# Performance work log

Hardware: AMD Instinct MI355X
Metric: run time of the kernel (lower is better)

The kernel has to match this reference:

```python
import jax, jax.numpy as jnp
import numpy as np

ROLE_BITS = 20
NHEAD = 16
D_MODEL = 1024
D_KEY = D_MODEL // NHEAD  # 64
D_FIL = 512
DFF = 4096
EPS = 1e-5


def _ln(x, g, b):
    mu = jnp.mean(x, axis=-1, keepdims=True)
    var = jnp.mean(jnp.square(x - mu), axis=-1, keepdims=True)
    return (x - mu) * jax.lax.rsqrt(var + EPS) * g + b


def setup_inputs() -> dict:
    key = jax.random.key(0)
    ks = jax.random.split(key, 10)
    N, BSZ, MEM = 16384, 16, 8
    D_IN = D_FIL + ROLE_BITS  # 532
    values = jax.random.normal(ks[0], (N, D_FIL), jnp.float32)
    role_index = jax.random.randint(ks[1], (N,), 1, 2 ** ROLE_BITS)
    # every (batch, memory_slot) pair occupied -> static shapes (compression is a no-op)
    slot = jax.random.permutation(ks[2], jnp.tile(jnp.arange(BSZ * MEM), N // (BSZ * MEM)))
    batch_index = (slot // MEM).astype(jnp.int32)
    memory_index = (slot % MEM).astype(jnp.int32)
    query_vectors = jax.random.normal(ks[3], (NHEAD, D_KEY), jnp.float32) * (1.0 / np.sqrt(D_KEY))
    s = 0.02
    Wk = jax.random.normal(ks[4], (D_MODEL, D_IN), jnp.float32) * s
    Wv = jax.random.normal(ks[5], (D_MODEL, D_IN), jnp.float32) * s
    Wo = jax.random.normal(ks[6], (D_MODEL, D_MODEL), jnp.float32) * s
    W1 = jax.random.normal(ks[7], (DFF, D_MODEL), jnp.float32) * s
    W2 = jax.random.normal(ks[8], (D_MODEL, DFF), jnp.float32) * s
    return dict(
        values=values, role_index=role_index, batch_index=batch_index,
        memory_index=memory_index, query_vectors=query_vectors,
        Wk=Wk, Wv=Wv, Wo=Wo, bo=jnp.zeros((D_MODEL,), jnp.float32),
        W1=W1, b1=jnp.zeros((DFF,), jnp.float32),
        W2=W2, b2=jnp.zeros((D_MODEL,), jnp.float32),
        g_fil=jnp.ones((D_FIL,), jnp.float32), b_fil=jnp.zeros((D_FIL,), jnp.float32),
        g_mha=jnp.ones((D_IN,), jnp.float32), b_mha=jnp.zeros((D_IN,), jnp.float32),
        g_ff=jnp.ones((D_MODEL,), jnp.float32), b_ff=jnp.zeros((D_MODEL,), jnp.float32),
        g_out=jnp.ones((D_MODEL,), jnp.float32), b_out=jnp.zeros((D_MODEL,), jnp.float32),
        bsz=BSZ, memory_slots=MEM,
    )


def _tree_positional_encodings(role_index):
    # bit-expand role indices: column j is bit j of the role index
    bits = (jnp.bitwise_and(role_index[:, None], 2 ** jnp.arange(ROLE_BITS)) != 0).astype(jnp.float32)
    # locate the highest set bit (torch: flip + argmax)
    mi = jnp.argmax(bits[:, ::-1], axis=1)
    cm = ROLE_BITS - 1 - mi  # index of highest set bit
    bits = bits * (1.0 - jax.nn.one_hot(cm, ROLE_BITS, dtype=bits.dtype))  # zero it out
    branch = jnp.arange(ROLE_BITS)[None, :] < cm[:, None]
    return jnp.where(branch, (bits - 0.5) * 2.0, bits)  # {0,1} -> {-1,1} below MSB


def reference(values, role_index, batch_index, memory_index, query_vectors,
              Wk, Wv, Wo, bo, W1, b1, W2, b2,
              g_fil, b_fil, g_mha, b_mha, g_ff, b_ff, g_out, b_out,
              bsz, memory_slots):
    N = values.shape[0]
    T = bsz * memory_slots  # num_trees (all (batch, slot) pairs occupied)

    tpd = _tree_positional_encodings(role_index)
    x = jnp.concatenate([_ln(values, g_fil, b_fil), tpd], axis=1)  # [N, d_input]
    x = _ln(x, g_mha, b_mha)
    k = (x @ Wk.T).reshape(N, NHEAD, D_KEY)
    v = (x @ Wv.T).reshape(N, NHEAD, D_KEY)
    qkm = jnp.einsum('nhd,hd->nh', k, query_vectors)  # [N, H]

    # combined batch+memory mask: node n attends to flat tree t = b*mem + m
    node_slot = batch_index * memory_slots + memory_index  # [N]
    mask = node_slot[:, None] == jnp.arange(T)[None, :]  # [N, T]
    scores = jnp.where(mask[:, :, None], qkm[:, None, :], -1e9) / np.sqrt(D_KEY)
    attn = jax.nn.softmax(scores, axis=0)  # softmax over nodes, [N, T, H]
    out = jnp.einsum('nhv,nth->thv', v, attn).reshape(T, D_MODEL)

    # post-attention: proj_o + residual with flattened queries, LN, FF, LN
    r1 = (out @ Wo.T + bo) + query_vectors.reshape(-1)
    l1 = _ln(r1, g_ff, b_ff)
    ff = jax.nn.gelu(l1 @ W1.T + b1, approximate=False) @ W2.T + b2
    l2 = _ln(ff + r1, g_out, b_out)

    rectangle_out = l2.reshape(bsz, memory_slots, D_MODEL)
    agent_pad_mask = jnp.zeros((bsz, memory_slots), dtype=bool)
    return rectangle_out, agent_pad_mask
```

## Files before the change

kernel.cpp:

```cpp
#include <hip/hip_runtime.h>
#include <hip/hip_bf16.h>

typedef __hip_bfloat16 bf16;

#define N_NODES 16384
#define D_FIL 512
#define D_IN 532
#define D_MODEL 1024
#define NHEAD 16
#define D_KEY 64
#define DFF 4096
#define NTREE 128
#define MEM_SLOTS 8
#define NODES_PER_TREE 128
#define EPS 1e-5f
#define XSE 544
#define XSU 272
#define CSTR 32
#define BSTR 40

typedef float f32x4 __attribute__((ext_vector_type(4)));
typedef short s16x8 __attribute__((ext_vector_type(8)));

union PackU { uint4 u; s16x8 s; };

__device__ inline float gelu_exact(float x) {
    return 0.5f * x * (1.0f + erff(x * 0.7071067811865476f));
}

__device__ inline void blockReduceSum2(float& a, float& b, float* sm) {
    int tid = threadIdx.x;
    int lane = tid & 63, wid = tid >> 6;
#pragma unroll
    for (int off = 32; off > 0; off >>= 1) {
        a += __shfl_down(a, off, 64);
        b += __shfl_down(b, off, 64);
    }
    if (lane == 0) { sm[wid] = a; sm[4 + wid] = b; }
    __syncthreads();
    if (tid == 0) {
        sm[8] = sm[0] + sm[1] + sm[2] + sm[3];
        sm[9] = sm[4] + sm[5] + sm[6] + sm[7];
    }
    __syncthreads();
    a = sm[8]; b = sm[9];
}

__global__ __launch_bounds__(256) void prep_kernel(
        const float* __restrict__ values, const int* __restrict__ role,
        const int* __restrict__ bidx, const int* __restrict__ midx,
        const float* __restrict__ g_fil, const float* __restrict__ b_fil,
        const float* __restrict__ g_mha, const float* __restrict__ b_mha,
        bf16* __restrict__ xs, int* __restrict__ counts,
        const float* __restrict__ q, const float* __restrict__ Wk,
        unsigned* __restrict__ wqb,
        const float* __restrict__ Wv, float* __restrict__ wvt) {
    int b = blockIdx.x;
    int tid = threadIdx.x;

    if (b < 16) {
        int h = b;
        __shared__ float qs[64];
        if (tid < 64) qs[tid] = q[h * 64 + tid];
        __syncthreads();
        for (int p = tid; p < XSU; p += 256) {
            unsigned out = 0u;
            if (p < 266) {
                float a0 = 0.f, a1 = 0.f;
                int j0 = 2 * p;
#pragma unroll 8
                for (int d = 0; d < 64; ++d) {
                    const float* wr = Wk + (size_t)(h * 64 + d) * D_IN;
                    a0 += qs[d] * wr[j0];
                    a1 += qs[d] * wr[j0 + 1];
                }
                unsigned u0 = (unsigned)__bfloat16_as_ushort(__float2bfloat16(a0));
                unsigned u1 = (unsigned)__bfloat16_as_ushort(__float2bfloat16(a1));
                out = (u1 << 16) | u0;
            }
            wqb[h * XSU + p] = out;
        }
        return;
    }

    if (b < 560) {
        __shared__ float tile[32][33];
        int vb = b - 16;
        int c0 = (vb & 31) * 32, j0 = (vb >> 5) * 32;
        int tx = tid & 31, ty = tid >> 5;
#pragma unroll
        for (int r = 0; r < 4; ++r) {
            int cc = ty + r * 8;
            int j = j0 + tx;
            tile[cc][tx] = (j < D_IN) ? Wv[(size_t)(c0 + cc) * D_IN + j] : 0.f;
        }
        __syncthreads();
#pragma unroll
        for (int r = 0; r < 4; ++r) {
            int j = j0 + ty + r * 8;
            if (j < D_IN) wvt[(size_t)j * D_MODEL + c0 + tx] = tile[tx][ty + r * 8];
        }
        return;
    }

    int wave = tid >> 6;
    int l = tid & 63;
    int n = (b - 560) * 4 + wave;

    const float4* vp = (const float4*)(values + (size_t)n * D_FIL + l * 8);
    float4 v0 = vp[0], v1 = vp[1];

    int row = 0;
    if (l == 0) {
        int slot = bidx[n] * MEM_SLOTS + midx[n];
        int pos = atomicAdd(&counts[slot * CSTR], 1);
        row = slot * NODES_PER_TREE + pos;
    }

    float s = v0.x + v0.y + v0.z + v0.w + v1.x + v1.y + v1.z + v1.w;
    float ss = v0.x * v0.x + v0.y * v0.y + v0.z * v0.z + v0.w * v0.w
             + v1.x * v1.x + v1.y * v1.y + v1.z * v1.z + v1.w * v1.w;
#pragma unroll
    for (int m = 1; m < 64; m <<= 1) {
        s += __shfl_xor(s, m, 64);
        ss += __shfl_xor(ss, m, 64);
    }
    float mu = s * (1.f / D_FIL);
    float var = ss * (1.f / D_FIL) - mu * mu;
    float rs = rsqrtf(var + EPS);

    const float4* gf = (const float4*)(g_fil + l * 8);
    const float4* bf = (const float4*)(b_fil + l * 8);
    float4 gf0 = gf[0], gf1 = gf[1], bf0 = bf[0], bf1 = bf[1];
    float y[8];
    y[0] = (v0.x - mu) * rs * gf0.x + bf0.x;
    y[1] = (v0.y - mu) * rs * gf0.y + bf0.y;
    y[2] = (v0.z - mu) * rs * gf0.z + bf0.z;
    y[3] = (v0.w - mu) * rs * gf0.w + bf0.w;
    y[4] = (v1.x - mu) * rs * gf1.x + bf1.x;
    y[5] = (v1.y - mu) * rs * gf1.y + bf1.y;
    y[6] = (v1.z - mu) * rs * gf1.z + bf1.z;
    y[7] = (v1.w - mu) * rs * gf1.w + bf1.w;

    int r = role[n];
    int cm = 31 - __clz(r);
    float s_t = 2.f * (float)(__popc(r) - 1) - (float)cm;
    float ss_t = (float)cm;

    float s2 = y[0] + y[1] + y[2] + y[3] + y[4] + y[5] + y[6] + y[7];
    float ss2 = y[0] * y[0] + y[1] * y[1] + y[2] * y[2] + y[3] * y[3]
              + y[4] * y[4] + y[5] * y[5] + y[6] * y[6] + y[7] * y[7];
#pragma unroll
    for (int m = 1; m < 64; m <<= 1) {
        s2 += __shfl_xor(s2, m, 64);
        ss2 += __shfl_xor(ss2, m, 64);
    }
    s2 += s_t; ss2 += ss_t;
    float mu2 = s2 * (1.f / D_IN);
    float var2 = ss2 * (1.f / D_IN) - mu2 * mu2;
    float rs2 = rsqrtf(var2 + EPS);

    const float4* gm = (const float4*)(g_mha + l * 8);
    const float4* bm = (const float4*)(b_mha + l * 8);
    float4 gm0 = gm[0], gm1 = gm[1], bm0 = bm[0], bm1 = bm[1];
    float x[8];
    x[0] = (y[0] - mu2) * rs2 * gm0.x + bm0.x;
    x[1] = (y[1] - mu2) * rs2 * gm0.y + bm0.y;
    x[2] = (y[2] - mu2) * rs2 * gm0.z + bm0.z;
    x[3] = (y[3] - mu2) * rs2 * gm0.w + bm0.w;
    x[4] = (y[4] - mu2) * rs2 * gm1.x + bm1.x;
    x[5] = (y[5] - mu2) * rs2 * gm1.y + bm1.y;
    x[6] = (y[6] - mu2) * rs2 * gm1.z + bm1.z;
    x[7] = (y[7] - mu2) * rs2 * gm1.w + bm1.w;

    row = __shfl(row, 0, 64);

    {
        unsigned us[8];
#pragma unroll
        for (int k = 0; k < 8; ++k)
            us[k] = (unsigned)__bfloat16_as_ushort(__float2bfloat16(x[k]));
        uint4 pk = make_uint4((us[1] << 16) | us[0], (us[3] << 16) | us[2],
                              (us[5] << 16) | us[4], (us[7] << 16) | us[6]);
        *(uint4*)((char*)xs + (size_t)row * (XSE * 2) + 16 * l) = pk;
    }

    if (l < 20) {
        int bit = (r >> l) & 1;
        float tpd = (l < cm) ? (bit ? 1.f : -1.f) : 0.f;
        float x2 = (tpd - mu2) * rs2 * g_mha[512 + l] + b_mha[512 + l];
        xs[(size_t)row * XSE + 512 + l] = __float2bfloat16(x2);
    } else if (l < 26) {
        ((unsigned*)xs)[(size_t)row * XSU + 266 + (l - 20)] = 0u;
    }
}

__global__ __launch_bounds__(256) void qkm_kernel(const unsigned* __restrict__ xsu,
                                                  const unsigned* __restrict__ wqb,
                                                  float* __restrict__ qkmp) {
    __shared__ unsigned wshw[16 * 274];
    int tid = threadIdx.x;
#pragma unroll
    for (int hh = 0; hh < 16; ++hh) {
        wshw[hh * 274 + tid] = wqb[hh * XSU + tid];
        if (tid < 16) wshw[hh * 274 + 256 + tid] = wqb[hh * XSU + 256 + tid];
    }
    __syncthreads();

    int h = tid & 15, rp = tid >> 4;
    int r0 = blockIdx.x * 32;
    const uint2* xr0 = (const uint2*)(xsu + (size_t)(r0 + 2 * rp) * XSU);
    const uint2* xr1 = (const uint2*)(xsu + (size_t)(r0 + 2 * rp + 1) * XSU);
    const uint2* wr  = (const uint2*)(wshw + h * 274);
    float a0 = 0.f, a1 = 0.f;
#pragma unroll 8
    for (int j = 0; j < 136; ++j) {
        uint2 wu = wr[j];
        uint2 xa = xr0[j];
        uint2 xb = xr1[j];
        float w0 = __uint_as_float(wu.x << 16), w1 = __uint_as_float(wu.x & 0xffff0000u);
        float w2 = __uint_as_float(wu.y << 16), w3 = __uint_as_float(wu.y & 0xffff0000u);
        a0 += __uint_as_float(xa.x << 16) * w0 + __uint_as_float(xa.x & 0xffff0000u) * w1
            + __uint_as_float(xa.y << 16) * w2 + __uint_as_float(xa.y & 0xffff0000u) * w3;
        a1 += __uint_as_float(xb.x << 16) * w0 + __uint_as_float(xb.x & 0xffff0000u) * w1
            + __uint_as_float(xb.y << 16) * w2 + __uint_as_float(xb.y & 0xffff0000u) * w3;
    }
    qkmp[(size_t)(r0 + 2 * rp) * NHEAD + h] = a0;
    qkmp[(size_t)(r0 + 2 * rp + 1) * NHEAD + h] = a1;
}

__global__ void attn_fused_kernel(const float* __restrict__ qkmp, const unsigned* __restrict__ xsu,
                                  const float* __restrict__ wvt, float* __restrict__ attn_out) {
    int hg = blockIdx.x, t = blockIdx.y, tid = threadIdx.x;
    __shared__ __align__(16) float a4[NODES_PER_TREE * 4];
    __shared__ float zs[4][536];

    for (int l = tid; l < NODES_PER_TREE * 4; l += 256) {
        int i = l >> 2, hh = l & 3;
        a4[l] = qkmp[(size_t)t * NODES_PER_TREE * NHEAD + i * 16 + hg * 4 + hh] * 0.125f;
    }
    __syncthreads();

    int hh = tid >> 6, lane = tid & 63;
    {
        float s0 = a4[lane * 4 + hh], s1 = a4[(lane + 64) * 4 + hh];
        float m = fmaxf(s0, s1);
#pragma unroll
        for (int off = 32; off > 0; off >>= 1) m = fmaxf(m, __shfl_xor(m, off, 64));
        float e0 = expf(s0 - m), e1 = expf(s1 - m);
        float sum = e0 + e1;
#pragma unroll
        for (int off = 32; off > 0; off >>= 1) sum += __shfl_xor(sum, off, 64);
        float inv = 1.0f / sum;
        a4[lane * 4 + hh] = e0 * inv;
        a4[(lane + 64) * 4 + hh] = e1 * inv;
    }
    __syncthreads();

    {
        bool hasT = tid < 10;
        float az[4][2] = {};
        float at[4][2] = {};
        const unsigned* xt = xsu + (size_t)t * NODES_PER_TREE * XSU;
        for (int i0 = 0; i0 < NODES_PER_TREE; i0 += 8) {
            unsigned u[8], u2[8];
            float4 av[8];
#pragma unroll
            for (int k = 0; k < 8; ++k) u[k] = xt[(size_t)(i0 + k) * XSU + tid];
#pragma unroll
            for (int k = 0; k < 8; ++k) u2[k] = hasT ? xt[(size_t)(i0 + k) * XSU + 256 + tid] : 0u;
#pragma unroll
            for (int k = 0; k < 8; ++k) av[k] = *(const float4*)(a4 + (i0 + k) * 4);
#pragma unroll
            for (int k = 0; k < 8; ++k) {
                float x0 = __uint_as_float(u[k] << 16);
                float x1 = __uint_as_float(u[k] & 0xffff0000u);
                float x2 = __uint_as_float(u2[k] << 16);
                float x3 = __uint_as_float(u2[k] & 0xffff0000u);
                float4 a = av[k];
                az[0][0] += a.x * x0; az[0][1] += a.x * x1;
                az[1][0] += a.y * x0; az[1][1] += a.y * x1;
                az[2][0] += a.z * x0; az[2][1] += a.z * x1;
                az[3][0] += a.w * x0; az[3][1] += a.w * x1;
                at[0][0] += a.x * x2; at[0][1] += a.x * x3;
                at[1][0] += a.y * x2; at[1][1] += a.y * x3;
                at[2][0] += a.z * x2; at[2][1] += a.z * x3;
                at[3][0] += a.w * x2; at[3][1] += a.w * x3;
            }
        }
#pragma unroll
        for (int k = 0; k < 4; ++k) {
            *(float2*)(&zs[k][2 * tid]) = make_float2(az[k][0], az[k][1]);
            if (hasT) *(float2*)(&zs[k][512 + 2 * tid]) = make_float2(at[k][0], at[k][1]);
        }
    }
    __syncthreads();

    int c = hg * 256 + tid;
    const float* wp = wvt + c;
    float acc0 = 0.f, acc1 = 0.f;
    for (int j0 = 0; j0 < 528; j0 += 8) {
        float wv[8];
#pragma unroll
        for (int k = 0; k < 8; ++k) wv[k] = wp[(size_t)(j0 + k) * D_MODEL];
#pragma unroll
        for (int k = 0; k < 8; k += 2) {
            acc0 += zs[hh][j0 + k] * wv[k];
            acc1 += zs[hh][j0 + k + 1] * wv[k + 1];
        }
    }
    {
        float wv[4];
#pragma unroll
        for (int k = 0; k < 4; ++k) wv[k] = wp[(size_t)(528 + k) * D_MODEL];
#pragma unroll
        for (int k = 0; k < 4; k += 2) {
            acc0 += zs[hh][528 + k] * wv[k];
            acc1 += zs[hh][528 + k + 1] * wv[k + 1];
        }
    }
    attn_out[(size_t)t * D_MODEL + c] = acc0 + acc1;
}

__global__ __launch_bounds__(256) void gemm_mfma_sk(const float* __restrict__ A,
                                                    const float* __restrict__ B,
                                                    float* __restrict__ Cpart,
                                                    int N, int K, int nsb) {
    __shared__ __align__(16) unsigned short bhi[64 * BSTR];
    __shared__ __align__(16) unsigned short blo[64 * BSTR];
    int tid = threadIdx.x;
    int col0 = blockIdx.x * 64;
    int k0 = blockIdx.y * nsb * 32;
    float* C = Cpart + (size_t)blockIdx.y * 128 * N;

    int w = tid >> 6, l = tid & 63;
    int l15 = l & 15, l4 = l >> 4;
    int scol = tid >> 2, sk8 = (tid & 3) * 8;

    f32x4 acc[2][4];
#pragma unroll
    for (int rt = 0; rt < 2; ++rt)
#pragma unroll
        for (int ct = 0; ct < 4; ++ct) acc[rt][ct] = (f32x4){0.f, 0.f, 0.f, 0.f};

    for (int s = 0; s < nsb; ++s) {
        int kb = k0 + s * 32;

        {
            const float* bp = B + (size_t)(col0 + scol) * K + kb + sk8;
            float4 f0 = *(const float4*)bp;
            float4 f1 = *(const float4*)(bp + 4);
            float fe[8] = {f0.x, f0.y, f0.z, f0.w, f1.x, f1.y, f1.z, f1.w};
            unsigned hu[4], lu[4];
#pragma unroll
            for (int p = 0; p < 4; ++p) {
                unsigned u0 = __float_as_uint(fe[2 * p]);
                unsigned u1 = __float_as_uint(fe[2 * p + 1]);
                unsigned h0 = u0 & 0xffff0000u, h1 = u1 & 0xffff0000u;
                float d0 = fe[2 * p] - __uint_as_float(h0);
                float d1 = fe[2 * p + 1] - __uint_as_float(h1);
                hu[p] = h1 | (u0 >> 16);
                lu[p] = (__float_as_uint(d1) & 0xffff0000u) | (__float_as_uint(d0) >> 16);
            }
            *(uint4*)(&bhi[scol * BSTR + sk8]) = make_uint4(hu[0], hu[1], hu[2], hu[3]);
            *(uint4*)(&blo[scol * BSTR + sk8]) = make_uint4(lu[0], lu[1], lu[2], lu[3]);
        }
        __syncthreads();

        s16x8 ah[2], al[2];
#pragma unroll
        for (int rt = 0; rt < 2; ++rt) {
            const float* ap = A + (size_t)(32 * w + 16 * rt + l15) * K + kb + l4 * 8;
            float4 f0 = *(const float4*)ap;
            float4 f1 = *(const float4*)(ap + 4);
            float fe[8] = {f0.x, f0.y, f0.z, f0.w, f1.x, f1.y, f1.z, f1.w};
            unsigned hu[4], lu[4];
#pragma unroll
            for (int p = 0; p < 4; ++p) {
                unsigned u0 = __float_as_uint(fe[2 * p]);
                unsigned u1 = __float_as_uint(fe[2 * p + 1]);
                unsigned h0 = u0 & 0xffff0000u, h1 = u1 & 0xffff0000u;
                float d0 = fe[2 * p] - __uint_as_float(h0);
                float d1 = fe[2 * p + 1] - __uint_as_float(h1);
                hu[p] = h1 | (u0 >> 16);
                lu[p] = (__float_as_uint(d1) & 0xffff0000u) | (__float_as_uint(d0) >> 16);
            }
            PackU uh, ul;
            uh.u = make_uint4(hu[0], hu[1], hu[2], hu[3]);
            ul.u = make_uint4(lu[0], lu[1], lu[2], lu[3]);
            ah[rt] = uh.s;
            al[rt] = ul.s;
        }

#pragma unroll
        for (int ct = 0; ct < 4; ++ct) {
            PackU rbh, rbl;
            rbh.u = *(const uint4*)(&bhi[(16 * ct + l15) * BSTR + l4 * 8]);
            rbl.u = *(const uint4*)(&blo[(16 * ct + l15) * BSTR + l4 * 8]);
#pragma unroll
            for (int rt = 0; rt < 2; ++rt) {
                acc[rt][ct] = __builtin_amdgcn_mfma_f32_16x16x32_bf16(ah[rt], rbh.s, acc[rt][ct], 0, 0, 0);
                acc[rt][ct] = __builtin_amdgcn_mfma_f32_16x16x32_bf16(al[rt], rbh.s, acc[rt][ct], 0, 0, 0);
                acc[rt][ct] = __builtin_amdgcn_mfma_f32_16x16x32_bf16(ah[rt], rbl.s, acc[rt][ct], 0, 0, 0);
            }
        }
        __syncthreads();
    }

#pragma unroll
    for (int rt = 0; rt < 2; ++rt) {
        int row = 32 * w + 16 * rt + l4 * 4;
#pragma unroll
        for (int ct = 0; ct < 4; ++ct) {
            int col = col0 + 16 * ct + l15;
#pragma unroll
            for (int r = 0; r < 4; ++r)
                C[(size_t)(row + r) * N + col] = acc[rt][ct][r];
        }
    }
}

__global__ void ln_r1_kernel(const float* __restrict__ po, const float* __restrict__ bo,
                             const float* __restrict__ qvec, const float* __restrict__ g,
                             const float* __restrict__ b, float* __restrict__ r1,
                             float* __restrict__ l1) {
    int t = blockIdx.x, tid = threadIdx.x;
    __shared__ float sm[16];
    float e[4];
#pragma unroll
    for (int c = 0; c < 4; ++c) {
        int j = c * 256 + tid;
        float v = bo[j] + qvec[j];
#pragma unroll
        for (int s = 0; s < 8; ++s)
            v += po[(size_t)s * NTREE * D_MODEL + (size_t)t * D_MODEL + j];
        e[c] = v;
        r1[(size_t)t * D_MODEL + j] = v;
    }
    float s = e[0] + e[1] + e[2] + e[3];
    float ss = e[0] * e[0] + e[1] * e[1] + e[2] * e[2] + e[3] * e[3];
    blockReduceSum2(s, ss, sm);
    float mu = s * (1.f / D_MODEL);
    float var = ss * (1.f / D_MODEL) - mu * mu;
    float rs = rsqrtf(var + EPS);
#pragma unroll
    for (int c = 0; c < 4; ++c) {
        int j = c * 256 + tid;
        l1[(size_t)t * D_MODEL + j] = (e[c] - mu) * rs * g[j] + b[j];
    }
}

__global__ void gelu_reduce_kernel(const float* __restrict__ p1, const float* __restrict__ b1,
                                   float* __restrict__ h1) {
    int idx4 = (blockIdx.x * 256 + threadIdx.x) * 4;
    int col = idx4 & (DFF - 1);
    float4 v = *(const float4*)(b1 + col);
#pragma unroll
    for (int s = 0; s < 4; ++s) {
        float4 p = *(const float4*)(p1 + (size_t)s * NTREE * DFF + idx4);
        v.x += p.x; v.y += p.y; v.z += p.z; v.w += p.w;
    }
    v.x = gelu_exact(v.x); v.y = gelu_exact(v.y);
    v.z = gelu_exact(v.z); v.w = gelu_exact(v.w);
    *(float4*)(h1 + idx4) = v;
}

__global__ void ln_out_kernel(const float* __restrict__ p2, const float* __restrict__ b2,
                              const float* __restrict__ r1, const float* __restrict__ g,
                              const float* __restrict__ b, float* __restrict__ out) {
    int t = blockIdx.x, tid = threadIdx.x;
    __shared__ float sm[16];
    float e[4];
#pragma unroll
    for (int c = 0; c < 4; ++c) {
        int j = c * 256 + tid;
        float v = b2[j] + r1[(size_t)t * D_MODEL + j];
#pragma unroll
        for (int s = 0; s < 16; ++s)
            v += p2[(size_t)s * NTREE * D_MODEL + (size_t)t * D_MODEL + j];
        e[c] = v;
    }
    float s = e[0] + e[1] + e[2] + e[3];
    float ss = e[0] * e[0] + e[1] * e[1] + e[2] * e[2] + e[3] * e[3];
    blockReduceSum2(s, ss, sm);
    float mu = s * (1.f / D_MODEL);
    float var = ss * (1.f / D_MODEL) - mu * mu;
    float rs = rsqrtf(var + EPS);
#pragma unroll
    for (int c = 0; c < 4; ++c) {
        int j = c * 256 + tid;
        out[(size_t)t * D_MODEL + j] = (e[c] - mu) * rs * g[j] + b[j];
    }
    if (t == 0 && tid < 128) out[(size_t)NTREE * D_MODEL + tid] = 0.f;
}

extern "C" void kernel_launch(void* const* d_in, const int* in_sizes, int n_in,
                              void* d_out, int out_size, void* d_ws, size_t ws_size,
                              hipStream_t stream) {
    const float* values = (const float*)d_in[0];
    const int* role     = (const int*)d_in[1];
    const int* bidx     = (const int*)d_in[2];
    const int* midx     = (const int*)d_in[3];
    const float* qvec   = (const float*)d_in[4];
    const float* Wk     = (const float*)d_in[5];
    const float* Wv     = (const float*)d_in[6];
    const float* Wo     = (const float*)d_in[7];
    const float* bo     = (const float*)d_in[8];
    const float* W1     = (const float*)d_in[9];
    const float* b1     = (const float*)d_in[10];
    const float* W2     = (const float*)d_in[11];
    const float* b2     = (const float*)d_in[12];
    const float* g_fil  = (const float*)d_in[13];
    const float* b_fil  = (const float*)d_in[14];
    const float* g_mha  = (const float*)d_in[15];
    const float* b_mha  = (const float*)d_in[16];
    const float* g_ff   = (const float*)d_in[17];
    const float* b_ff   = (const float*)d_in[18];
    const float* g_out  = (const float*)d_in[19];
    const float* b_out  = (const float*)d_in[20];

    char* w = (char*)d_ws;
    unsigned* wqb   = (unsigned*)(w + 0);
    float* qkmp     = (float*)(w + 18432);
    float* attn_out = (float*)(w + 1068032);
    float* r1       = (float*)(w + 1592320);
    float* l1       = (float*)(w + 2116608);
    float* h1       = (float*)(w + 2640896);
    int*   counts   = (int*)  (w + 2640896);
    float* wvt      = (float*)(w + 4738048);
    char*  big      = w + 6917120;
    bf16*  xs = (bf16*)big;
    float* po = (float*)big;
    float* p1 = (float*)(big + 4194304);
    float* p2 = (float*)big;

    float* out = (float*)d_out;

    hipMemsetAsync(counts, 0, 128 * CSTR * sizeof(int), stream);

    prep_kernel<<<4656, 256, 0, stream>>>(values, role, bidx, midx,
                                          g_fil, b_fil, g_mha, b_mha,
                                          xs, counts,
                                          qvec, Wk, wqb, Wv, wvt);

    qkm_kernel<<<N_NODES / 32, 256, 0, stream>>>((const unsigned*)xs, wqb, qkmp);

    attn_fused_kernel<<<dim3(4, NTREE), 256, 0, stream>>>(qkmp, (const unsigned*)xs, wvt, attn_out);

    gemm_mfma_sk<<<dim3(16, 8), 256, 0, stream>>>(attn_out, Wo, po, D_MODEL, D_MODEL, 4);

    ln_r1_kernel<<<NTREE, 256, 0, stream>>>(po, bo, qvec, g_ff, b_ff, r1, l1);

    gemm_mfma_sk<<<dim3(64, 4), 256, 0, stream>>>(l1, W1, p1, DFF, D_MODEL, 8);

    gelu_reduce_kernel<<<512, 256, 0, stream>>>(p1, b1, h1);

    gemm_mfma_sk<<<dim3(16, 16), 256, 0, stream>>>(h1, W2, p2, D_MODEL, DFF, 8);

    ln_out_kernel<<<NTREE, 256, 0, stream>>>(p2, b2, r1, g_out, b_out, out);
}
```

Baseline: 243.4 us.

## Halve GEMM column tile, double grid, hoist loads, widen LayerNorm blocks

The split-K MFMA GEMM now computes 32-column tiles instead of 64, so each of the three post-attention GEMMs launches twice as many blocks. This spreads the small M=128 GEMMs across more compute units, at the cost of reloading and re-splitting the A tile once per extra block. The A and B global loads are also issued before the bf16 hi/lo split and the LDS store, so their latency can overlap. The two LayerNorm kernels move to 512 threads per row with a matching 8-wave reduction.

```diff
diff --git a/kernel.cpp b/kernel.cpp
--- a/kernel.cpp
+++ b/kernel.cpp
@@ -28,7 +28,7 @@
     return 0.5f * x * (1.0f + erff(x * 0.7071067811865476f));
 }
 
-__device__ inline void blockReduceSum2(float& a, float& b, float* sm) {
+__device__ inline void blockReduceSum2_512(float& a, float& b, float* sm) {
     int tid = threadIdx.x;
     int lane = tid & 63, wid = tid >> 6;
 #pragma unroll
@@ -36,14 +36,16 @@
         a += __shfl_down(a, off, 64);
         b += __shfl_down(b, off, 64);
     }
-    if (lane == 0) { sm[wid] = a; sm[4 + wid] = b; }
+    if (lane == 0) { sm[wid] = a; sm[8 + wid] = b; }
     __syncthreads();
     if (tid == 0) {
-        sm[8] = sm[0] + sm[1] + sm[2] + sm[3];
-        sm[9] = sm[4] + sm[5] + sm[6] + sm[7];
+        float s0 = 0.f, s1 = 0.f;
+#pragma unroll
+        for (int i = 0; i < 8; ++i) { s0 += sm[i]; s1 += sm[8 + i]; }
+        sm[16] = s0; sm[17] = s1;
     }
     __syncthreads();
-    a = sm[8]; b = sm[9];
+    a = sm[16]; b = sm[17];
 }
 
 __global__ __launch_bounds__(256) void prep_kernel(
@@ -326,34 +328,42 @@
                                                     const float* __restrict__ B,
                                                     float* __restrict__ Cpart,
                                                     int N, int K, int nsb) {
-    __shared__ __align__(16) unsigned short bhi[64 * BSTR];
-    __shared__ __align__(16) unsigned short blo[64 * BSTR];
+    __shared__ __align__(16) unsigned short bhi[32 * BSTR];
+    __shared__ __align__(16) unsigned short blo[32 * BSTR];
     int tid = threadIdx.x;
-    int col0 = blockIdx.x * 64;
+    int col0 = blockIdx.x * 32;
     int k0 = blockIdx.y * nsb * 32;
     float* C = Cpart + (size_t)blockIdx.y * 128 * N;
 
     int w = tid >> 6, l = tid & 63;
     int l15 = l & 15, l4 = l >> 4;
-    int scol = tid >> 2, sk8 = (tid & 3) * 8;
-
-    f32x4 acc[2][4];
+    int scol = tid >> 3, sk4 = (tid & 7) * 4;
+
+    f32x4 acc[2][2];
 #pragma unroll
     for (int rt = 0; rt < 2; ++rt)
 #pragma unroll
-        for (int ct = 0; ct < 4; ++ct) acc[rt][ct] = (f32x4){0.f, 0.f, 0.f, 0.f};
+        for (int ct = 0; ct < 2; ++ct) acc[rt][ct] = (f32x4){0.f, 0.f, 0.f, 0.f};
 
     for (int s = 0; s < nsb; ++s) {
         int kb = k0 + s * 32;
 
+        const float* bp = B + (size_t)(col0 + scol) * K + kb + sk4;
+        float4 fb = *(const float4*)bp;
+
+        float4 fa[2][2];
+#pragma unroll
+        for (int rt = 0; rt < 2; ++rt) {
+            const float* ap = A + (size_t)(32 * w + 16 * rt + l15) * K + kb + l4 * 8;
+            fa[rt][0] = *(const float4*)ap;
+            fa[rt][1] = *(const float4*)(ap + 4);
+        }
+
         {
-            const float* bp = B + (size_t)(col0 + scol) * K + kb + sk8;
-            float4 f0 = *(const float4*)bp;
-            float4 f1 = *(const float4*)(bp + 4);
-            float fe[8] = {f0.x, f0.y, f0.z, f0.w, f1.x, f1.y, f1.z, f1.w};
-            unsigned hu[4], lu[4];
-#pragma unroll
-            for (int p = 0; p < 4; ++p) {
+            float fe[4] = {fb.x, fb.y, fb.z, fb.w};
+            unsigned hu[2], lu[2];
+#pragma unroll
+            for (int p = 0; p < 2; ++p) {
                 unsigned u0 = __float_as_uint(fe[2 * p]);
                 unsigned u1 = __float_as_uint(fe[2 * p + 1]);
                 unsigned h0 = u0 & 0xffff0000u, h1 = u1 & 0xffff0000u;
@@ -362,18 +372,16 @@
                 hu[p] = h1 | (u0 >> 16);
                 lu[p] = (__float_as_uint(d1) & 0xffff0000u) | (__float_as_uint(d0) >> 16);
             }
-            *(uint4*)(&bhi[scol * BSTR + sk8]) = make_uint4(hu[0], hu[1], hu[2], hu[3]);
-            *(uint4*)(&blo[scol * BSTR + sk8]) = make_uint4(lu[0], lu[1], lu[2], lu[3]);
+            *(uint2*)(&bhi[scol * BSTR + sk4]) = make_uint2(hu[0], hu[1]);
+            *(uint2*)(&blo[scol * BSTR + sk4]) = make_uint2(lu[0], lu[1]);
         }
         __syncthreads();
 
         s16x8 ah[2], al[2];
 #pragma unroll
         for (int rt = 0; rt < 2; ++rt) {
-            const float* ap = A + (size_t)(32 * w + 16 * rt + l15) * K + kb + l4 * 8;
-            float4 f0 = *(const float4*)ap;
-            float4 f1 = *(const float4*)(ap + 4);
-            float fe[8] = {f0.x, f0.y, f0.z, f0.w, f1.x, f1.y, f1.z, f1.w};
+            float fe[8] = {fa[rt][0].x, fa[rt][0].y, fa[rt][0].z, fa[rt][0].w,
+                           fa[rt][1].x, fa[rt][1].y, fa[rt][1].z, fa[rt][1].w};
             unsigned hu[4], lu[4];
 #pragma unroll
             for (int p = 0; p < 4; ++p) {
@@ -393,7 +401,7 @@
         }
 
 #pragma unroll
-        for (int ct = 0; ct < 4; ++ct) {
+        for (int ct = 0; ct < 2; ++ct) {
             PackU rbh, rbl;
             rbh.u = *(const uint4*)(&bhi[(16 * ct + l15) * BSTR + l4 * 8]);
             rbl.u = *(const uint4*)(&blo[(16 * ct + l15) * BSTR + l4 * 8]);
@@ -411,7 +419,7 @@
     for (int rt = 0; rt < 2; ++rt) {
         int row = 32 * w + 16 * rt + l4 * 4;
 #pragma unroll
-        for (int ct = 0; ct < 4; ++ct) {
+        for (int ct = 0; ct < 2; ++ct) {
             int col = col0 + 16 * ct + l15;
 #pragma unroll
             for (int r = 0; r < 4; ++r)
@@ -420,16 +428,16 @@
     }
 }
 
-__global__ void ln_r1_kernel(const float* __restrict__ po, const float* __restrict__ bo,
+__global__ __launch_bounds__(512) void ln_r1_kernel(const float* __restrict__ po, const float* __restrict__ bo,
                              const float* __restrict__ qvec, const float* __restrict__ g,
                              const float* __restrict__ b, float* __restrict__ r1,
                              float* __restrict__ l1) {
     int t = blockIdx.x, tid = threadIdx.x;
-    __shared__ float sm[16];
-    float e[4];
-#pragma unroll
-    for (int c = 0; c < 4; ++c) {
-        int j = c * 256 + tid;
+    __shared__ float sm[18];
+    float e[2];
+#pragma unroll
+    for (int c = 0; c < 2; ++c) {
+        int j = c * 512 + tid;
         float v = bo[j] + qvec[j];
 #pragma unroll
         for (int s = 0; s < 8; ++s)
@@ -437,15 +445,15 @@
         e[c] = v;
         r1[(size_t)t * D_MODEL + j] = v;
     }
-    float s = e[0] + e[1] + e[2] + e[3];
-    float ss = e[0] * e[0] + e[1] * e[1] + e[2] * e[2] + e[3] * e[3];
-    blockReduceSum2(s, ss, sm);
+    float s = e[0] + e[1];
+    float ss = e[0] * e[0] + e[1] * e[1];
+    blockReduceSum2_512(s, ss, sm);
     float mu = s * (1.f / D_MODEL);
     float var = ss * (1.f / D_MODEL) - mu * mu;
     float rs = rsqrtf(var + EPS);
 #pragma unroll
-    for (int c = 0; c < 4; ++c) {
-        int j = c * 256 + tid;
+    for (int c = 0; c < 2; ++c) {
+        int j = c * 512 + tid;
         l1[(size_t)t * D_MODEL + j] = (e[c] - mu) * rs * g[j] + b[j];
     }
 }
@@ -465,30 +473,30 @@
     *(float4*)(h1 + idx4) = v;
 }
 
-__global__ void ln_out_kernel(const float* __restrict__ p2, const float* __restrict__ b2,
+__global__ __launch_bounds__(512) void ln_out_kernel(const float* __restrict__ p2, const float* __restrict__ b2,
                               const float* __restrict__ r1, const float* __restrict__ g,
                               const float* __restrict__ b, float* __restrict__ out) {
     int t = blockIdx.x, tid = threadIdx.x;
-    __shared__ float sm[16];
-    float e[4];
-#pragma unroll
-    for (int c = 0; c < 4; ++c) {
-        int j = c * 256 + tid;
+    __shared__ float sm[18];
+    float e[2];
+#pragma unroll
+    for (int c = 0; c < 2; ++c) {
+        int j = c * 512 + tid;
         float v = b2[j] + r1[(size_t)t * D_MODEL + j];
 #pragma unroll
         for (int s = 0; s < 16; ++s)
             v += p2[(size_t)s * NTREE * D_MODEL + (size_t)t * D_MODEL + j];
         e[c] = v;
     }
-    float s = e[0] + e[1] + e[2] + e[3];
-    float ss = e[0] * e[0] + e[1] * e[1] + e[2] * e[2] + e[3] * e[3];
-    blockReduceSum2(s, ss, sm);
+    float s = e[0] + e[1];
+    float ss = e[0] * e[0] + e[1] * e[1];
+    blockReduceSum2_512(s, ss, sm);
     float mu = s * (1.f / D_MODEL);
     float var = ss * (1.f / D_MODEL) - mu * mu;
     float rs = rsqrtf(var + EPS);
 #pragma unroll
-    for (int c = 0; c < 4; ++c) {
-        int j = c * 256 + tid;
+    for (int c = 0; c < 2; ++c) {
+        int j = c * 512 + tid;
         out[(size_t)t * D_MODEL + j] = (e[c] - mu) * rs * g[j] + b[j];
     }
     if (t == 0 && tid < 128) out[(size_t)NTREE * D_MODEL + tid] = 0.f;
@@ -547,15 +555,15 @@
 
     attn_fused_kernel<<<dim3(4, NTREE), 256, 0, stream>>>(qkmp, (const unsigned*)xs, wvt, attn_out);
 
-    gemm_mfma_sk<<<dim3(16, 8), 256, 0, stream>>>(attn_out, Wo, po, D_MODEL, D_MODEL, 4);
-
-    ln_r1_kernel<<<NTREE, 256, 0, stream>>>(po, bo, qvec, g_ff, b_ff, r1, l1);
-
-    gemm_mfma_sk<<<dim3(64, 4), 256, 0, stream>>>(l1, W1, p1, DFF, D_MODEL, 8);
+    gemm_mfma_sk<<<dim3(32, 8), 256, 0, stream>>>(attn_out, Wo, po, D_MODEL, D_MODEL, 4);
+
+    ln_r1_kernel<<<NTREE, 512, 0, stream>>>(po, bo, qvec, g_ff, b_ff, r1, l1);
+
+    gemm_mfma_sk<<<dim3(128, 4), 256, 0, stream>>>(l1, W1, p1, DFF, D_MODEL, 8);
 
     gelu_reduce_kernel<<<512, 256, 0, stream>>>(p1, b1, h1);
 
-    gemm_mfma_sk<<<dim3(16, 16), 256, 0, stream>>>(h1, W2, p2, D_MODEL, DFF, 8);
-
-    ln_out_kernel<<<NTREE, 256, 0, stream>>>(p2, b2, r1, g_out, b_out, out);
-}
+    gemm_mfma_sk<<<dim3(32, 16), 256, 0, stream>>>(h1, W2, p2, D_MODEL, DFF, 8);
+
+    ln_out_kernel<<<NTREE, 512, 0, stream>>>(p2, b2, r1, g_out, b_out, out);
+}
```

After: 240.6 us. Within noise of the previous version (-1.1%).
